# Performance work log

Measured on AMD Instinct MI355X. Metric: run time of the kernel, lower is better.

## Reference

```python
import jax, jax.numpy as jnp
import numpy as np

DIMBED = 1024
DIMLAT = 1024
SEQ = 2048
BATCH = 16
LN_EPS = float(DIMBED)  # quirk: nn.LayerNorm(BATCH_SIZE, dimbed) -> eps = dimbed


def setup_inputs() -> dict:
    key = jax.random.key(0)
    ks = jax.random.split(key, 8)
    s_in = 1.0 / np.sqrt(DIMBED)
    s_lat = 1.0 / np.sqrt(DIMLAT)
    return {
        "x": jax.random.normal(ks[0], (SEQ, DIMBED, BATCH), dtype=jnp.float32),
        "Wq": jax.random.normal(ks[1], (DIMLAT, DIMBED), dtype=jnp.float32) * s_in,
        "Wk": jax.random.normal(ks[2], (DIMLAT, DIMBED), dtype=jnp.float32) * s_in,
        "Wv": jax.random.normal(ks[3], (DIMLAT, DIMBED), dtype=jnp.float32) * s_in,
        "Wg": jax.random.normal(ks[4], (DIMBED, DIMLAT), dtype=jnp.float32) * s_lat,
        "bg": jax.random.normal(ks[5], (DIMBED,), dtype=jnp.float32) * 0.01,
        "ln_w": jnp.ones((BATCH,), dtype=jnp.float32),
        "ln_b": jnp.zeros((BATCH,), dtype=jnp.float32),
    }


def reference(x, Wq, Wk, Wv, Wg, bg, ln_w, ln_b):
    # LayerNorm over last axis (size BATCH=16), eps = dimbed (faithful quirk)
    mu = jnp.mean(x, axis=-1, keepdims=True)
    var = jnp.mean(jnp.square(x - mu), axis=-1, keepdims=True)
    xt = (x - mu) * jax.lax.rsqrt(var + LN_EPS) * ln_w + ln_b  # (S, D, B)

    xt2 = jnp.transpose(xt, (0, 2, 1))  # (S, B, D) -- x.transpose(1,2)
    q = jnp.einsum('sbd,ld->sbl', xt2, Wq)  # (S, B, L)
    k = jnp.einsum('sbd,ld->sbl', xt2, Wk)
    v = jnp.einsum('sbd,ld->sbl', xt2, Wv)

    # e[b,s,t] = sum_l q[s,b,l] * k[t,b,l]
    e = jnp.einsum('sbl,tbl->bst', q, k)  # (B, S, S)
    # softmax over dim=1 (the query axis s), scaled by 1/sqrt(dimbed)
    a = jax.nn.softmax(e / np.sqrt(DIMBED).astype(np.float32), axis=1)
    ftheta = jnp.einsum('bst,tbl->bsl', a, v)  # (B, S, L)

    out = jnp.einsum('bsl,dl->bsd', ftheta, Wg) + bg  # (B, S, D)
    return jnp.transpose(out, (1, 2, 0))  # (S, D, B)
```

## Files before the change

kernel.cpp:

```cpp
#include <hip/hip_runtime.h>
#include <hip/hip_bf16.h>
#include <stdint.h>

using bf16 = __hip_bfloat16;
typedef __attribute__((ext_vector_type(4))) float f32x4;
typedef __attribute__((ext_vector_type(8))) short s16x8;
typedef __attribute__((ext_vector_type(4))) short s16x4;

#define SEQN 2048
#define DIMD 1024
#define NB   16

#define GLDS16(gp, lp)                                                      \
  __builtin_amdgcn_global_load_lds(                                         \
      (const __attribute__((address_space(1))) void*)(gp),                  \
      (__attribute__((address_space(3))) void*)(lp), 16, 0, 0)

__global__ void cvt_kernel(const float* __restrict__ Wq, const float* __restrict__ Wk,
                           const float* __restrict__ Wv, const float* __restrict__ Wg,
                           bf16* __restrict__ Wqkv, bf16* __restrict__ Wgb) {
  const int i = blockIdx.x * 256 + threadIdx.x;
  const int which = blockIdx.y;
  const float* src = (which == 0) ? Wq : (which == 1) ? Wk : (which == 2) ? Wv : Wg;
  bf16* dst = (which < 3) ? (Wqkv + (size_t)which * DIMD * DIMD) : Wgb;
  f32x4 f = ((const f32x4*)src)[i];
  s16x4 pack;
#pragma unroll
  for (int j = 0; j < 4; ++j) {
    bf16 t = __float2bfloat16(f[j]);
    pack[j] = *reinterpret_cast<short*>(&t);
  }
  *reinterpret_cast<s16x4*>(dst + (size_t)i * 4) = pack;
}

__global__ void ln_kernel(const float* __restrict__ x, const float* __restrict__ lnw,
                          const float* __restrict__ lnb, bf16* __restrict__ xt) {
  const int idx = blockIdx.x * 256 + threadIdx.x;
  const int s = idx >> 10, d = idx & 1023;
  const float4* xp = reinterpret_cast<const float4*>(x + (size_t)idx * NB);
  float v[16];
#pragma unroll
  for (int j = 0; j < 4; ++j) reinterpret_cast<float4*>(v)[j] = xp[j];
  float mu = 0.f;
#pragma unroll
  for (int j = 0; j < 16; ++j) mu += v[j];
  mu *= (1.f / 16.f);
  float var = 0.f;
#pragma unroll
  for (int j = 0; j < 16; ++j) { float t = v[j] - mu; var += t * t; }
  var *= (1.f / 16.f);
  const float inv = rsqrtf(var + 1024.0f);
#pragma unroll
  for (int b = 0; b < 16; ++b) {
    float o = (v[b] - mu) * inv * lnw[b] + lnb[b];
    xt[((size_t)b * SEQN + s) * DIMD + d] = __float2bfloat16(o);
  }
}

template <int MODE>
__global__ __launch_bounds__(512, 2)
void gemm256(const bf16* __restrict__ Ag, const bf16* __restrict__ Bg,
             bf16* __restrict__ C, float* __restrict__ Cf,
             const float* __restrict__ bias,
             const int K, const int lda, const int ldb, const size_t ldc,
             const size_t sA, const size_t sB, const size_t sC,
             const int tn, const float escale) {
  __shared__ bf16 sm[4][2][256 * 32];

  const int nwg = gridDim.x;
  const int flat = blockIdx.x;
  const int tile = (flat & 7) * (nwg >> 3) + (flat >> 3);
  const int m0 = (tile / tn) * 256;
  const int n0 = (tile % tn) * 256;

  const int bz = blockIdx.z;
  const bf16* A = Ag + (size_t)bz * sA;
  const bf16* B = Bg + (size_t)bz * sB;
  const size_t coff = (size_t)bz * sC;

  const int tid = threadIdx.x;
  const int w = tid >> 6;
  const int lane = tid & 63;
  const int wr = w >> 2, wc = w & 3;
  const int r16 = lane & 15, hi = lane >> 4;

  const int srow = tid >> 2;
  const int scol = ((tid & 3) * 8) ^ (((srow >> 3) & 1) << 4);
  const bf16* gA0 = A + (size_t)(m0 + srow) * lda + scol;
  const bf16* gA1 = A + (size_t)(m0 + 128 + srow) * lda + scol;
  const bf16* gB0 = B + (size_t)(n0 + srow) * ldb + scol;
  const bf16* gB1 = B + (size_t)(n0 + 128 + srow) * ldb + scol;
  const int wbase = w * 512;

  const int fcol = (hi * 8) ^ (((r16 >> 3) & 1) << 4);
  const int aoff = (wr * 128 + r16) * 32 + fcol;
  const int boff = (wc * 64 + r16) * 32 + fcol;

  f32x4 acc[8][4] = {};
  const int NT = K >> 5;

#define STAGE(tt, bb) do {                                                  \
    const int k0_ = (tt) << 5;                                              \
    bf16* sA_ = &sm[bb][0][0];                                              \
    bf16* sB_ = &sm[bb][1][0];                                              \
    GLDS16(gA0 + k0_, sA_ + wbase);                                         \
    GLDS16(gA1 + k0_, sA_ + 4096 + wbase);                                  \
    GLDS16(gB0 + k0_, sB_ + wbase);                                         \
    GLDS16(gB1 + k0_, sB_ + 4096 + wbase);                                  \
  } while (0)

#define COMPUTE(bb) do {                                                    \
    const bf16* pA_ = &sm[bb][0][aoff];                                     \
    const bf16* pB_ = &sm[bb][1][boff];                                     \
    s16x8 af[8], bfr[4];                                                    \
    _Pragma("unroll")                                                       \
    for (int mf = 0; mf < 8; ++mf) af[mf] = *(const s16x8*)(pA_ + mf * 512);\
    _Pragma("unroll")                                                       \
    for (int nf = 0; nf < 4; ++nf) bfr[nf] = *(const s16x8*)(pB_ + nf * 512);\
    __builtin_amdgcn_s_setprio(1);                                          \
    _Pragma("unroll")                                                       \
    for (int mf = 0; mf < 8; ++mf)                                          \
      _Pragma("unroll")                                                     \
      for (int nf = 0; nf < 4; ++nf)                                        \
        acc[mf][nf] = __builtin_amdgcn_mfma_f32_16x16x32_bf16(af[mf], bfr[nf], acc[mf][nf], 0, 0, 0); \
    __builtin_amdgcn_s_setprio(0);                                          \
  } while (0)

#define BAR() asm volatile("s_barrier" ::: "memory")
#define VMW(n) asm volatile("s_waitcnt vmcnt(" #n ")" ::: "memory")

  STAGE(0, 0);
  STAGE(1, 1);
  STAGE(2, 2);

  int t = 0;
  for (; t < NT - 3; ++t) {
    STAGE(t + 3, (t + 3) & 3);
    VMW(12);
    BAR();
    COMPUTE(t & 3);
    BAR();
  }
  VMW(8);  BAR(); COMPUTE(t & 3); ++t;
  VMW(4);  BAR(); COMPUTE(t & 3); ++t;
  VMW(0);  BAR(); COMPUTE(t & 3);

#undef STAGE
#undef COMPUTE
#undef BAR
#undef VMW

#pragma unroll
  for (int mf = 0; mf < 8; ++mf) {
#pragma unroll
    for (int nf = 0; nf < 4; ++nf) {
      f32x4 v = acc[mf][nf];
      const int gm0 = m0 + wr * 128 + mf * 16 + hi * 4;
      const int gn = n0 + wc * 64 + nf * 16 + r16;
#pragma unroll
      for (int i = 0; i < 4; ++i) {
        const int gm = gm0 + i;
        if (MODE == 0) {
          C[coff + (size_t)gm * ldc + gn] = __float2bfloat16(v[i]);
        } else if (MODE == 1) {
          C[coff + (size_t)gm * ldc + gn] = __float2bfloat16(__expf(v[i] * escale));
        } else {
          Cf[((size_t)(gm >> 4)) * (DIMD * NB) + (size_t)gn * NB + (gm & 15)] = v[i] + bias[gn];
        }
      }
    }
  }
}

__global__ void colsum_kernel(const bf16* __restrict__ p, float* __restrict__ Zp) {
  const int tcol = blockIdx.x * 256 + threadIdx.x;
  const int b = blockIdx.y;
  const int ch = blockIdx.z;
  const bf16* pp = p + ((size_t)b * SEQN + ch * 256) * SEQN + tcol;
  float s = 0.f;
#pragma unroll 8
  for (int i = 0; i < 256; ++i) s += __bfloat162float(pp[(size_t)i * SEQN]);
  Zp[((size_t)ch * NB + b) * SEQN + tcol] = s;
}

__global__ void zinv_kernel(const float* __restrict__ Zp, float* __restrict__ Zinv) {
  const int i = blockIdx.x * 256 + threadIdx.x;
  float s = 0.f;
#pragma unroll
  for (int c = 0; c < 8; ++c) s += Zp[(size_t)c * (NB * SEQN) + i];
  Zinv[i] = 1.0f / s;
}

__global__ void vtrans_kernel(const bf16* __restrict__ QKV, const float* __restrict__ Zinv,
                              bf16* __restrict__ vpp) {
  __shared__ bf16 tile[64][66];
  const int b = blockIdx.z;
  const int t0 = blockIdx.x * 64;
  const int l0 = blockIdx.y * 64;
  const int tid = threadIdx.x;
  const int col = tid & 63, rw = tid >> 6;
#pragma unroll
  for (int i = 0; i < 16; ++i) {
    const int r = i * 4 + rw;
    tile[r][col] = QKV[((size_t)b * SEQN + t0 + r) * 3072 + 2048 + l0 + col];
  }
  __syncthreads();
  const float z = Zinv[b * SEQN + t0 + col];
#pragma unroll
  for (int i = 0; i < 16; ++i) {
    const int lr = i * 4 + rw;
    vpp[((size_t)b * DIMD + l0 + lr) * SEQN + t0 + col] =
        __float2bfloat16(__bfloat162float(tile[col][lr]) * z);
  }
}

extern "C" void kernel_launch(void* const* d_in, const int* in_sizes, int n_in,
                              void* d_out, int out_size, void* d_ws, size_t ws_size,
                              hipStream_t stream) {
  const float* x   = (const float*)d_in[0];
  const float* Wq  = (const float*)d_in[1];
  const float* Wk  = (const float*)d_in[2];
  const float* Wv  = (const float*)d_in[3];
  const float* Wg  = (const float*)d_in[4];
  const float* bg  = (const float*)d_in[5];
  const float* lnw = (const float*)d_in[6];
  const float* lnb = (const float*)d_in[7];
  float* out = (float*)d_out;

  char* ws = (char*)d_ws;
  size_t off = 0;
  auto alloc = [&](size_t bytes) {
    char* p = ws + off;
    off += (bytes + 255) & ~(size_t)255;
    return p;
  };
  bf16* Wqkv = (bf16*)alloc((size_t)3072 * DIMD * 2);
  bf16* Wgb  = (bf16*)alloc((size_t)DIMD * DIMD * 2);
  bf16* xt   = (bf16*)alloc((size_t)NB * SEQN * DIMD * 2);
  bf16* QKV  = (bf16*)alloc((size_t)NB * SEQN * 3072 * 2);
  bf16* p    = (bf16*)alloc((size_t)NB * SEQN * SEQN * 2);
  float* Zp  = (float*)alloc((size_t)8 * NB * SEQN * 4);
  float* Zinv = (float*)alloc((size_t)NB * SEQN * 4);
  bf16* vpp = xt;
  bf16* fth = QKV;

  const dim3 blk(256);
  const dim3 blk512(512);

  cvt_kernel<<<dim3(1024, 4), blk, 0, stream>>>(Wq, Wk, Wv, Wg, Wqkv, Wgb);
  ln_kernel<<<dim3(SEQN * DIMD / 256), blk, 0, stream>>>(x, lnw, lnb, xt);
  gemm256<0><<<dim3(128 * 12, 1, 1), blk512, 0, stream>>>(
      xt, Wqkv, QKV, nullptr, nullptr,
       DIMD,  DIMD,  DIMD,  3072,
      0, 0, 0,  12, 0.f);
  gemm256<1><<<dim3(8 * 8, 1, 16), blk512, 0, stream>>>(
      QKV, QKV + 1024, p, nullptr, nullptr,
       DIMD,  3072,  3072,  SEQN,
      (size_t)SEQN * 3072, (size_t)SEQN * 3072, (size_t)SEQN * SEQN,  8, 0.03125f);
  colsum_kernel<<<dim3(8, 16, 8), blk, 0, stream>>>(p, Zp);
  zinv_kernel<<<dim3(NB * SEQN / 256), blk, 0, stream>>>(Zp, Zinv);
  vtrans_kernel<<<dim3(32, 16, 16), blk, 0, stream>>>(QKV, Zinv, vpp);
  gemm256<0><<<dim3(8 * 4, 1, 16), blk512, 0, stream>>>(
      p, vpp, fth, nullptr, nullptr,
       SEQN,  SEQN,  SEQN,  (size_t)NB * DIMD,
      (size_t)SEQN * SEQN, (size_t)DIMD * SEQN, DIMD,  4, 0.f);
  gemm256<2><<<dim3(128 * 4, 1, 1), blk512, 0, stream>>>(
      fth, Wgb, nullptr, out, bg,
       DIMD,  DIMD,  DIMD,  0,
      0, 0, 0,  4, 0.f);
}
```

Baseline: 885.3 us.

## Restructure GEMM mainloop to 64-wide K tiles with quadrant-interleaved double buffering

The 256x256 bf16 GEMM now loads 64-wide K tiles into two LDS buffers instead of 32-wide tiles into four. It uses a new XOR swizzle over 8-element groups. Each K tile is split into four MFMA quadrants, and each quadrant's LDS fragment reads and next-tile global-to-LDS loads are interleaved with the others, separated by barriers. The aim is finer overlap of loads with MFMA work and fewer LDS bank conflicts, at the cost of many more barriers per iteration and a shallower prefetch depth.

Result: faster. 860.3 us (-2.8%).

```diff
diff --git a/kernel.cpp b/kernel.cpp
--- a/kernel.cpp
+++ b/kernel.cpp
@@ -65,7 +65,7 @@
              const int K, const int lda, const int ldb, const size_t ldc,
              const size_t sA, const size_t sB, const size_t sC,
              const int tn, const float escale) {
-  __shared__ bf16 sm[4][2][256 * 32];
+  __shared__ bf16 sm[2][2][16384];
 
   const int nwg = gridDim.x;
   const int flat = blockIdx.x;
@@ -83,70 +83,98 @@
   const int lane = tid & 63;
   const int wr = w >> 2, wc = w & 3;
   const int r16 = lane & 15, hi = lane >> 4;
-
-  const int srow = tid >> 2;
-  const int scol = ((tid & 3) * 8) ^ (((srow >> 3) & 1) << 4);
-  const bf16* gA0 = A + (size_t)(m0 + srow) * lda + scol;
-  const bf16* gA1 = A + (size_t)(m0 + 128 + srow) * lda + scol;
-  const bf16* gB0 = B + (size_t)(n0 + srow) * ldb + scol;
-  const bf16* gB1 = B + (size_t)(n0 + 128 + srow) * ldb + scol;
-  const int wbase = w * 512;
-
-  const int fcol = (hi * 8) ^ (((r16 >> 3) & 1) << 4);
-  const int aoff = (wr * 128 + r16) * 32 + fcol;
-  const int boff = (wc * 64 + r16) * 32 + fcol;
+  const int xorb = r16 & 7;
+
+  const int slrow = tid >> 3;
+  const int sgrp = (tid & 7) ^ (slrow & 7);
+  const bf16* gSA = A + (size_t)(m0 + slrow) * lda + sgrp * 8;
+  const bf16* gSB = B + (size_t)(n0 + slrow) * ldb + sgrp * 8;
+  const int w512 = w * 512;
+
+  const int off0 = r16 * 64 + ((0 + hi) ^ xorb) * 8;
+  const int off1 = r16 * 64 + ((4 + hi) ^ xorb) * 8;
 
   f32x4 acc[8][4] = {};
-  const int NT = K >> 5;
-
-#define STAGE(tt, bb) do {                                                  \
-    const int k0_ = (tt) << 5;                                              \
-    bf16* sA_ = &sm[bb][0][0];                                              \
-    bf16* sB_ = &sm[bb][1][0];                                              \
-    GLDS16(gA0 + k0_, sA_ + wbase);                                         \
-    GLDS16(gA1 + k0_, sA_ + 4096 + wbase);                                  \
-    GLDS16(gB0 + k0_, sB_ + wbase);                                         \
-    GLDS16(gB1 + k0_, sB_ + 4096 + wbase);                                  \
+  s16x8 aF[4][2], bF[2][2];
+  const int NT = K >> 6;
+
+#define SQ_A(q, kt, bb)                                                      \
+  GLDS16(gSA + (size_t)((q) * 64) * lda + (size_t)(kt) * 64,                 \
+         &sm[bb][0][(q) * 4096 + w512])
+#define SQ_B(q, kt, bb)                                                      \
+  GLDS16(gSB + (size_t)((q) * 64) * ldb + (size_t)(kt) * 64,                 \
+         &sm[bb][1][(q) * 4096 + w512])
+
+#define READ_A(mh, bb) do {                                                  \
+    const bf16* pa_ = &sm[bb][0][(2 * wr + (mh)) * 4096];                    \
+    _Pragma("unroll")                                                        \
+    for (int sub = 0; sub < 4; ++sub) {                                      \
+      aF[sub][0] = *(const s16x8*)(pa_ + sub * 1024 + off0);                 \
+      aF[sub][1] = *(const s16x8*)(pa_ + sub * 1024 + off1);                 \
+    }                                                                        \
   } while (0)
 
-#define COMPUTE(bb) do {                                                    \
-    const bf16* pA_ = &sm[bb][0][aoff];                                     \
-    const bf16* pB_ = &sm[bb][1][boff];                                     \
-    s16x8 af[8], bfr[4];                                                    \
-    _Pragma("unroll")                                                       \
-    for (int mf = 0; mf < 8; ++mf) af[mf] = *(const s16x8*)(pA_ + mf * 512);\
-    _Pragma("unroll")                                                       \
-    for (int nf = 0; nf < 4; ++nf) bfr[nf] = *(const s16x8*)(pB_ + nf * 512);\
-    __builtin_amdgcn_s_setprio(1);                                          \
-    _Pragma("unroll")                                                       \
-    for (int mf = 0; mf < 8; ++mf)                                          \
-      _Pragma("unroll")                                                     \
-      for (int nf = 0; nf < 4; ++nf)                                        \
-        acc[mf][nf] = __builtin_amdgcn_mfma_f32_16x16x32_bf16(af[mf], bfr[nf], acc[mf][nf], 0, 0, 0); \
-    __builtin_amdgcn_s_setprio(0);                                          \
+#define READ_B(nh, bb) do {                                                  \
+    const bf16* pb_ = &sm[bb][1][wc * 4096 + (nh) * 2048];                   \
+    _Pragma("unroll")                                                        \
+    for (int j = 0; j < 2; ++j) {                                            \
+      bF[j][0] = *(const s16x8*)(pb_ + j * 1024 + off0);                     \
+      bF[j][1] = *(const s16x8*)(pb_ + j * 1024 + off1);                     \
+    }                                                                        \
+  } while (0)
+
+#define MFMA_Q(mh, nh) do {                                                  \
+    __builtin_amdgcn_s_setprio(1);                                           \
+    _Pragma("unroll")                                                        \
+    for (int k = 0; k < 2; ++k)                                              \
+      _Pragma("unroll")                                                      \
+      for (int j = 0; j < 2; ++j)                                            \
+        _Pragma("unroll")                                                    \
+        for (int sub = 0; sub < 4; ++sub)                                    \
+          acc[(mh) * 4 + sub][(nh) * 2 + j] = __builtin_amdgcn_mfma_f32_16x16x32_bf16( \
+              aF[sub][k], bF[j][k], acc[(mh) * 4 + sub][(nh) * 2 + j], 0, 0, 0); \
+    __builtin_amdgcn_s_setprio(0);                                           \
   } while (0)
 
 #define BAR() asm volatile("s_barrier" ::: "memory")
 #define VMW(n) asm volatile("s_waitcnt vmcnt(" #n ")" ::: "memory")
 
-  STAGE(0, 0);
-  STAGE(1, 1);
-  STAGE(2, 2);
+  SQ_B(0, 0, 0); SQ_B(1, 0, 0); SQ_B(2, 0, 0); SQ_B(3, 0, 0);
+  SQ_A(0, 0, 0); SQ_A(2, 0, 0); SQ_A(1, 0, 0); SQ_A(3, 0, 0);
+  VMW(2);
+  BAR();
 
   int t = 0;
-  for (; t < NT - 3; ++t) {
-    STAGE(t + 3, (t + 3) & 3);
-    VMW(12);
-    BAR();
-    COMPUTE(t & 3);
-    BAR();
-  }
-  VMW(8);  BAR(); COMPUTE(t & 3); ++t;
-  VMW(4);  BAR(); COMPUTE(t & 3); ++t;
-  VMW(0);  BAR(); COMPUTE(t & 3);
-
-#undef STAGE
-#undef COMPUTE
+  for (; t < NT - 1; ++t) {
+    const int cb = t & 1, nb = cb ^ 1, nk = t + 1;
+    READ_A(0, cb); READ_B(0, cb);
+    SQ_B(0, nk, nb); SQ_B(1, nk, nb);
+    BAR(); MFMA_Q(0, 0); BAR();
+    READ_B(1, cb);
+    SQ_B(2, nk, nb); SQ_B(3, nk, nb);
+    VMW(4);
+    BAR(); MFMA_Q(0, 1); BAR();
+    READ_A(1, cb); READ_B(0, cb);
+    SQ_A(0, nk, nb); SQ_A(2, nk, nb);
+    BAR(); MFMA_Q(1, 0); BAR();
+    READ_B(1, cb);
+    SQ_A(1, nk, nb); SQ_A(3, nk, nb);
+    VMW(2);
+    BAR(); MFMA_Q(1, 1); BAR();
+  }
+  {
+    const int cb = t & 1;
+    READ_A(0, cb); READ_B(0, cb); BAR(); MFMA_Q(0, 0); BAR();
+    READ_B(1, cb); VMW(0); BAR(); MFMA_Q(0, 1); BAR();
+    READ_A(1, cb); READ_B(0, cb); BAR(); MFMA_Q(1, 0); BAR();
+    READ_B(1, cb); BAR(); MFMA_Q(1, 1); BAR();
+  }
+
+#undef SQ_A
+#undef SQ_B
+#undef READ_A
+#undef READ_B
+#undef MFMA_Q
 #undef BAR
 #undef VMW
 
```
